# Performance work log

Measured on AMD Instinct MI355X. Metric: run time of the kernel, lower is better.

## Reference

```python
import jax, jax.numpy as jnp
import numpy as np
from jax import lax

PATCH = 16
TAU = 0.5
EPS = 1e-8  # torch CosineSimilarity default eps


def setup_inputs() -> dict:
    key = jax.random.key(0)
    k1, k2, k3, k4, k5 = jax.random.split(key, 5)
    B, C, HW = 64, 3, 384
    hidden, latent = 768, 1024
    return {
        "x": jax.random.normal(k1, (B, C, HW, HW), dtype=jnp.float32),
        "conv_w": jax.random.normal(k2, (hidden, C, PATCH, PATCH), dtype=jnp.float32) * 0.02,
        "conv_b": jax.random.normal(k3, (hidden,), dtype=jnp.float32) * 0.02,
        "latent1": jax.random.normal(k4, (1, latent, hidden), dtype=jnp.float32),
        "latent2": jax.random.normal(k5, (1, latent, hidden), dtype=jnp.float32),
    }


def _cosine_scores(p, p_norm, lat):
    # p: (B, N, D); lat: (L, D) -> (B, N, L) cosine similarity
    l_norm = jnp.linalg.norm(lat, axis=-1)  # (L,)
    dots = jnp.einsum('bnd,ld->bnl', p, lat)
    denom = jnp.maximum(p_norm[:, :, None] * l_norm[None, None, :], EPS)
    return dots / denom


def reference(x, conv_w, conv_b, latent1, latent2):
    # Patch embedding: Conv2d(kernel=stride=16, padding=0)
    patch = lax.conv_general_dilated(
        x, conv_w, window_strides=(PATCH, PATCH), padding='VALID',
        dimension_numbers=('NCHW', 'OIHW', 'NCHW'))
    patch = patch + conv_b[None, :, None, None]  # (B, D, H', W')
    B, D = patch.shape[0], patch.shape[1]
    p = patch.reshape(B, D, -1).transpose(0, 2, 1)  # (B, N, D)
    p_norm = jnp.linalg.norm(p, axis=-1)  # (B, N)

    far = _cosine_scores(p, p_norm, latent1[0])    # (B, N, L)
    close = _cosine_scores(p, p_norm, latent2[0])  # (B, N, L)

    sum_close = jnp.sum(jnp.exp(close / TAU), axis=(1, 2))  # (B,)
    sum_far = jnp.sum(jnp.exp(far / TAU), axis=(1, 2))      # (B,)
    loss = -jnp.log(sum_close / sum_far)
    return loss.mean()
```

## Files before the change

### kernel.cpp

```cpp
#include <hip/hip_runtime.h>
#include <math.h>

using f32x4  = __attribute__((ext_vector_type(4))) float;
using bf16x8 = __attribute__((ext_vector_type(8))) short;

typedef const __attribute__((address_space(1))) void gas_void;
typedef __attribute__((address_space(3))) void las_void;

__device__ __forceinline__ void gl16(const void* g, void* l) {
    __builtin_amdgcn_global_load_lds((gas_void*)g, (las_void*)l, 16, 0, 0);
}

__device__ __forceinline__ unsigned short f2bf(float f) {
    union { float f; unsigned u; } v; v.f = f;
    unsigned r = v.u + 0x7fffu + ((v.u >> 16) & 1u);
    return (unsigned short)(r >> 16);
}
__device__ __forceinline__ float bf2f(unsigned short u) {
    return __uint_as_float(((unsigned)u) << 16);
}

#define VW0() asm volatile("s_waitcnt vmcnt(0)")
#define BAR() __builtin_amdgcn_s_barrier()

__global__ void pcl_prep_wl(const float* __restrict__ w,
                            const float* __restrict__ l1, const float* __restrict__ l2,
                            unsigned short* __restrict__ wsW,
                            unsigned short* __restrict__ wsL) {
    int r = blockIdx.x, t = threadIdx.x;
    if (r < 768) {
        const float* src = w + (size_t)r * 768;
        unsigned short* dst = wsW + (size_t)r * 768;
#pragma unroll
        for (int i = 0; i < 12; ++i) dst[t + 64 * i] = f2bf(src[t + 64 * i]);
    } else {
        int lr = r - 768;
        const float* src = (lr < 1024) ? l1 + (size_t)lr * 768 : l2 + (size_t)(lr - 1024) * 768;
        unsigned short* dst = wsL + (size_t)lr * 768;
        float vals[12];
        float s = 0.f;
#pragma unroll
        for (int i = 0; i < 12; ++i) {
            float f = bf2f(f2bf(src[t + 64 * i]));
            vals[i] = f; s += f * f;
        }
#pragma unroll
        for (int off = 32; off; off >>= 1) s += __shfl_xor(s, off, 64);
        float rn = 1.0f / sqrtf(s);
#pragma unroll
        for (int i = 0; i < 12; ++i) dst[t + 64 * i] = f2bf(vals[i] * rn);
    }
}

#define K1_LDS 108544

__global__ __launch_bounds__(512, 1)
void pcl_k1(const float* __restrict__ x,
            const unsigned short* __restrict__ wsW,
            const float* __restrict__ bias,
            unsigned short* __restrict__ pbuf,
            float* __restrict__ rpn) {
    extern __shared__ char smem[];
    char* AA = smem;
    char* BB = smem + 8192;
    float* nrm = (float*)(smem + 106496);
    const int t = threadIdx.x, w = t >> 6, l = t & 63;
    const size_t Mb = (size_t)blockIdx.x * 64;
    const int ir = l >> 3, s2 = (l & 7) ^ ir;
    const int lm = l & 15, lg4 = l >> 4;

    const int sr = t >> 3, ss = t & 7;
    {
    }
    const int n = (int)Mb + sr;
    const int bb_ = n / 576, n5 = n % 576;
    const int ph = n5 / 24, pw = n5 % 24;
    const float* xbase = x + ((size_t)(bb_ * 3)) * 147456
                       + (size_t)(ph * 16 + (ss >> 1)) * 384 + pw * 16 + (ss & 1) * 8;
    char* aw = AA + sr * 128 + ((ss ^ (sr & 7)) << 4);

    f32x4 acc[4][6];
#pragma unroll
    for (int m = 0; m < 4; ++m)
#pragma unroll
        for (int nf = 0; nf < 6; ++nf) acc[m][nf] = (f32x4)0.f;

    f32x4 xr0, xr1;
    {
        const float* s = xbase;
        xr0 = *(const f32x4*)s; xr1 = *(const f32x4*)(s + 4);
    }

    for (int kc = 0; kc < 12; ++kc) {
        __syncthreads();
#pragma unroll
        for (int rep = 0; rep < 12; ++rep) {
            int c2 = w + 8 * rep;
            gl16(wsW + (size_t)(c2 * 8 + ir) * 768 + kc * 64 + s2 * 8, BB + c2 * 1024);
        }
        {
            bf16x8 pkt;
#pragma unroll
            for (int j = 0; j < 4; ++j) {
                pkt[j]     = (short)f2bf(xr0[j]);
                pkt[4 + j] = (short)f2bf(xr1[j]);
            }
            *(bf16x8*)aw = pkt;
        }
        __syncthreads();

        if (kc < 11) {
            int kn = kc + 1;
            const float* s = xbase + (size_t)(kn >> 2) * 147456 + (kn & 3) * 1536;
            xr0 = *(const f32x4*)s; xr1 = *(const f32x4*)(s + 4);
        }

        bf16x8 a[4][2];
#pragma unroll
        for (int m = 0; m < 4; ++m)
#pragma unroll
            for (int ks = 0; ks < 2; ++ks) {
                int r = m * 16 + lm, slot = ks * 4 + lg4;
                a[m][ks] = *(const bf16x8*)(AA + r * 128 + ((slot ^ (r & 7)) << 4));
            }
#pragma unroll
        for (int nf = 0; nf < 6; ++nf) {
            int rb = w * 96 + nf * 16 + lm;
#pragma unroll
            for (int ks = 0; ks < 2; ++ks) {
                int slot = ks * 4 + lg4;
                bf16x8 bb = *(const bf16x8*)(BB + rb * 128 + ((slot ^ (rb & 7)) << 4));
#pragma unroll
                for (int m = 0; m < 4; ++m)
                    acc[m][nf] = __builtin_amdgcn_mfma_f32_16x16x32_bf16(a[m][ks], bb, acc[m][nf], 0, 0, 0);
            }
        }
    }

    float rs[4][4];
#pragma unroll
    for (int m = 0; m < 4; ++m)
#pragma unroll
        for (int j = 0; j < 4; ++j) rs[m][j] = 0.f;
#pragma unroll
    for (int nf = 0; nf < 6; ++nf) {
        int d = w * 96 + nf * 16 + lm;
        float bv = bias[d];
#pragma unroll
        for (int m = 0; m < 4; ++m)
#pragma unroll
            for (int j = 0; j < 4; ++j) {
                int r = m * 16 + lg4 * 4 + j;
                unsigned short h = f2bf(acc[m][nf][j] + bv);
                pbuf[(Mb + r) * 768 + d] = h;
                float fv = bf2f(h);
                rs[m][j] += fv * fv;
            }
    }
#pragma unroll
    for (int m = 0; m < 4; ++m)
#pragma unroll
        for (int j = 0; j < 4; ++j) {
            rs[m][j] += __shfl_xor(rs[m][j], 1);
            rs[m][j] += __shfl_xor(rs[m][j], 2);
            rs[m][j] += __shfl_xor(rs[m][j], 4);
            rs[m][j] += __shfl_xor(rs[m][j], 8);
        }
    if (lm == 0) {
#pragma unroll
        for (int m = 0; m < 4; ++m)
#pragma unroll
            for (int j = 0; j < 4; ++j)
                nrm[(m * 16 + lg4 * 4 + j) * 8 + w] = rs[m][j];
    }
    __syncthreads();
    if (t < 64) {
        float s = 0.f;
#pragma unroll
        for (int i = 0; i < 8; ++i) s += nrm[t * 8 + i];
        rpn[Mb + t] = 1.0f / sqrtf(s);
    }
}

#define K2_LDS 81920

__global__ __launch_bounds__(256, 2)
void pcl_k2(const unsigned short* __restrict__ pbuf,
            const unsigned short* __restrict__ wsL,
            const float* __restrict__ rpn,
            double* __restrict__ partials) {
    extern __shared__ char smem[];
    const int t = threadIdx.x, w = t >> 6, l = t & 63;
    const int wg = (blockIdx.x & 7) * 384 + (blockIdx.x >> 3);
    const int mt = wg >> 4, nt = wg & 15;
    const size_t Mb = (size_t)mt * 192;
    const int Nb = nt * 128;
    const int wm = w >> 1, wn = w & 1;
    const int ir = l >> 3, s2 = (l & 7) ^ ir;
    const int lm = l & 15, lg4 = l >> 4;

    char* buf0 = smem;
    char* buf1 = smem + 40960;

    auto stage = [&](int kt, char* buf) {
#pragma unroll
        for (int rr = 0; rr < 6; ++rr) {
            int c2 = w * 6 + rr;
            gl16(pbuf + (Mb + c2 * 8 + ir) * 768 + kt * 64 + s2 * 8, buf + c2 * 1024);
        }
#pragma unroll
        for (int rr = 0; rr < 4; ++rr) {
            int c2 = w * 4 + rr;
            gl16(wsL + (size_t)(Nb + c2 * 8 + ir) * 768 + kt * 64 + s2 * 8,
                 buf + 24576 + c2 * 1024);
        }
    };

    f32x4 acc[6][4];
#pragma unroll
    for (int m = 0; m < 6; ++m)
#pragma unroll
        for (int nb = 0; nb < 4; ++nb) acc[m][nb] = (f32x4)0.f;

    stage(0, buf0);
    VW0(); BAR();

    bf16x8 areg[3][2], breg[4][2];

#pragma unroll 2
    for (int kt = 0; kt < 12; ++kt) {
        char* cur = (kt & 1) ? buf1 : buf0;
        char* nxt = (kt & 1) ? buf0 : buf1;

        if (kt < 11) stage(kt + 1, nxt);

#pragma unroll
        for (int nb = 0; nb < 4; ++nb)
#pragma unroll
            for (int ks = 0; ks < 2; ++ks) {
                int rb = wn * 64 + nb * 16 + lm, slot = ks * 4 + lg4;
                breg[nb][ks] = *(const bf16x8*)(cur + 24576 + rb * 128 + ((slot ^ (rb & 7)) << 4));
            }
#pragma unroll
        for (int m = 0; m < 3; ++m)
#pragma unroll
            for (int ks = 0; ks < 2; ++ks) {
                int r = wm * 96 + m * 16 + lm, slot = ks * 4 + lg4;
                areg[m][ks] = *(const bf16x8*)(cur + r * 128 + ((slot ^ (r & 7)) << 4));
            }
        __builtin_amdgcn_s_setprio(1);
#pragma unroll
        for (int m = 0; m < 3; ++m)
#pragma unroll
            for (int nb = 0; nb < 4; ++nb)
#pragma unroll
                for (int ks = 0; ks < 2; ++ks)
                    acc[m][nb] = __builtin_amdgcn_mfma_f32_16x16x32_bf16(areg[m][ks], breg[nb][ks], acc[m][nb], 0, 0, 0);
        __builtin_amdgcn_s_setprio(0);

#pragma unroll
        for (int m = 0; m < 3; ++m)
#pragma unroll
            for (int ks = 0; ks < 2; ++ks) {
                int r = wm * 96 + 48 + m * 16 + lm, slot = ks * 4 + lg4;
                areg[m][ks] = *(const bf16x8*)(cur + r * 128 + ((slot ^ (r & 7)) << 4));
            }
        __builtin_amdgcn_s_setprio(1);
#pragma unroll
        for (int m = 0; m < 3; ++m)
#pragma unroll
            for (int nb = 0; nb < 4; ++nb)
#pragma unroll
                for (int ks = 0; ks < 2; ++ks)
                    acc[3 + m][nb] = __builtin_amdgcn_mfma_f32_16x16x32_bf16(areg[m][ks], breg[nb][ks], acc[3 + m][nb], 0, 0, 0);
        __builtin_amdgcn_s_setprio(0);

        VW0();
        BAR();
    }

    double ssum = 0.0;
#pragma unroll
    for (int m = 0; m < 6; ++m) {
        int mh = m / 3, mi = m % 3;
        int rl = wm * 96 + mh * 48 + mi * 16;
        float rv[4];
#pragma unroll
        for (int j = 0; j < 4; ++j) rv[j] = rpn[Mb + rl + lg4 * 4 + j];
        float es = 0.f;
#pragma unroll
        for (int nb = 0; nb < 4; ++nb)
#pragma unroll
            for (int j = 0; j < 4; ++j)
                es += __expf(2.0f * acc[m][nb][j] * rv[j]);
        ssum += (double)es;
    }
#pragma unroll
    for (int off = 32; off; off >>= 1) ssum += __shfl_down(ssum, off);
    __syncthreads();
    double* red = (double*)smem;
    if (l == 0) red[w] = ssum;
    __syncthreads();
    if (t == 0) {
        double s = 0.0;
#pragma unroll
        for (int i = 0; i < 4; ++i) s += red[i];
        partials[wg] = s;
    }
}

__global__ void pcl_finish(const double* __restrict__ partials, float* __restrict__ out) {
    int b = threadIdx.x;
    double far = 0.0, close = 0.0;
#pragma unroll
    for (int i = 0; i < 3; ++i) {
        int mt = b * 3 + i;
#pragma unroll
        for (int nTile = 0; nTile < 16; ++nTile) {
            double v = partials[mt * 16 + nTile];
            if (nTile < 8) far += v; else close += v;
        }
    }
    double lb = log(far) - log(close);
#pragma unroll
    for (int off = 32; off; off >>= 1) lb += __shfl_down(lb, off);
    if (b == 0) out[0] = (float)(lb * (1.0 / 64.0));
}

extern "C" void kernel_launch(void* const* d_in, const int* in_sizes, int n_in,
                              void* d_out, int out_size, void* d_ws, size_t ws_size,
                              hipStream_t stream) {
    const float* x    = (const float*)d_in[0];
    const float* w    = (const float*)d_in[1];
    const float* bias = (const float*)d_in[2];
    const float* l1   = (const float*)d_in[3];
    const float* l2   = (const float*)d_in[4];
    float* out = (float*)d_out;

    unsigned short* pbuf = (unsigned short*)d_ws;
    unsigned short* wsW  = (unsigned short*)((char*)d_ws + 56623104);
    unsigned short* wsL  = (unsigned short*)((char*)d_ws + 57802752);
    float* rpn           = (float*)((char*)d_ws + 60948480);
    double* partials     = (double*)((char*)d_ws + 61095936);

    (void)hipFuncSetAttribute((const void*)pcl_k1,
                              hipFuncAttributeMaxDynamicSharedMemorySize, K1_LDS);
    (void)hipFuncSetAttribute((const void*)pcl_k2,
                              hipFuncAttributeMaxDynamicSharedMemorySize, K2_LDS);

    pcl_prep_wl<<<2816, 64, 0, stream>>>(w, l1, l2, wsW, wsL);
    pcl_k1<<<576, 512, K1_LDS, stream>>>(x, wsW, bias, pbuf, rpn);
    pcl_k2<<<3072, 256, K2_LDS, stream>>>(pbuf, wsL, rpn, partials);
    pcl_finish<<<1, 64, 0, stream>>>(partials, out);
}
```

Baseline: 216.8 us.

## Retile patch-embed GEMM into 192x128 double-buffered tiles with split norm reduction

The patch-embedding GEMM kernel now uses 192x128 output tiles on 256-thread blocks (two per CU) instead of 64x768 tiles on 512-thread blocks. It double-buffers the A and B tiles in LDS so the next k-step's global loads overlap the current MFMAs, and raises wave priority around the MFMA bursts. Because each block now covers only part of the hidden dimension, per-row squared norms are written as partials and reduced by a new small kernel. The aim is better occupancy and latency hiding for the conversion-heavy fp32 x loads. In exchange, each x element is now read and converted once per column tile (six times), and there is an extra launch.

```diff
diff --git a/kernel.cpp b/kernel.cpp
--- a/kernel.cpp
+++ b/kernel.cpp
@@ -21,6 +21,7 @@
 }
 
 #define VW0() asm volatile("s_waitcnt vmcnt(0)")
+#define VWL0() asm volatile("s_waitcnt vmcnt(0) lgkmcnt(0)")
 #define BAR() __builtin_amdgcn_s_barrier()
 
 __global__ void pcl_prep_wl(const float* __restrict__ w,
@@ -52,113 +53,167 @@
     }
 }
 
-#define K1_LDS 108544
-
-__global__ __launch_bounds__(512, 1)
+#define K1_LDS 81920
+
+__global__ __launch_bounds__(256, 2)
 void pcl_k1(const float* __restrict__ x,
             const unsigned short* __restrict__ wsW,
             const float* __restrict__ bias,
             unsigned short* __restrict__ pbuf,
-            float* __restrict__ rpn) {
+            float* __restrict__ rpnp) {
     extern __shared__ char smem[];
-    char* AA = smem;
-    char* BB = smem + 8192;
-    float* nrm = (float*)(smem + 106496);
     const int t = threadIdx.x, w = t >> 6, l = t & 63;
-    const size_t Mb = (size_t)blockIdx.x * 64;
+    const int wg = (blockIdx.x & 7) * 144 + (blockIdx.x >> 3);
+    const int mt = wg / 6, nt = wg % 6;
+    const size_t Mb = (size_t)mt * 192;
+    const int Nb = nt * 128;
+    const int wm = w >> 1, wn = w & 1;
     const int ir = l >> 3, s2 = (l & 7) ^ ir;
     const int lm = l & 15, lg4 = l >> 4;
 
-    const int sr = t >> 3, ss = t & 7;
-    {
-    }
-    const int n = (int)Mb + sr;
-    const int bb_ = n / 576, n5 = n % 576;
-    const int ph = n5 / 24, pw = n5 % 24;
-    const float* xbase = x + ((size_t)(bb_ * 3)) * 147456
-                       + (size_t)(ph * 16 + (ss >> 1)) * 384 + pw * 16 + (ss & 1) * 8;
-    char* aw = AA + sr * 128 + ((ss ^ (sr & 7)) << 4);
-
-    f32x4 acc[4][6];
-#pragma unroll
-    for (int m = 0; m < 4; ++m)
-#pragma unroll
-        for (int nf = 0; nf < 6; ++nf) acc[m][nf] = (f32x4)0.f;
-
-    f32x4 xr0, xr1;
-    {
-        const float* s = xbase;
-        xr0 = *(const f32x4*)s; xr1 = *(const f32x4*)(s + 4);
-    }
-
-    for (int kc = 0; kc < 12; ++kc) {
-        __syncthreads();
-#pragma unroll
-        for (int rep = 0; rep < 12; ++rep) {
-            int c2 = w + 8 * rep;
-            gl16(wsW + (size_t)(c2 * 8 + ir) * 768 + kc * 64 + s2 * 8, BB + c2 * 1024);
-        }
-        {
+    char* buf0 = smem;
+    char* buf1 = smem + 40960;
+
+    const int sl8 = t & 7;
+    const float* xbase[6];
+    int awoff[6];
+#pragma unroll
+    for (int rep = 0; rep < 6; ++rep) {
+        int row = rep * 32 + (t >> 3);
+        int n = (int)Mb + row;
+        int b = n / 576, n5 = n % 576;
+        int ph = n5 / 24, pw = n5 % 24;
+        xbase[rep] = x + (size_t)b * 442368 + (size_t)ph * 6144 + pw * 16;
+        awoff[rep] = row * 128 + ((sl8 ^ (row & 7)) << 4);
+    }
+    auto xoff = [&](int kt) {
+        int k0 = kt * 64 + sl8 * 8;
+        return (k0 >> 8) * 147456 + (((k0 >> 4) & 15)) * 384 + (k0 & 15);
+    };
+
+    auto issueB = [&](int kt, char* buf) {
+#pragma unroll
+        for (int rr = 0; rr < 4; ++rr) {
+            int c2 = w * 4 + rr;
+            gl16(wsW + (size_t)(Nb + c2 * 8 + ir) * 768 + kt * 64 + s2 * 8,
+                 buf + 24576 + c2 * 1024);
+        }
+    };
+
+    f32x4 xr[6][2];
+    auto loadX = [&](int kt) {
+        int off = xoff(kt);
+#pragma unroll
+        for (int rep = 0; rep < 6; ++rep) {
+            const float* s = xbase[rep] + off;
+            xr[rep][0] = *(const f32x4*)s;
+            xr[rep][1] = *(const f32x4*)(s + 4);
+        }
+    };
+    auto writeA = [&](char* buf) {
+#pragma unroll
+        for (int rep = 0; rep < 6; ++rep) {
             bf16x8 pkt;
 #pragma unroll
             for (int j = 0; j < 4; ++j) {
-                pkt[j]     = (short)f2bf(xr0[j]);
-                pkt[4 + j] = (short)f2bf(xr1[j]);
-            }
-            *(bf16x8*)aw = pkt;
-        }
-        __syncthreads();
-
-        if (kc < 11) {
-            int kn = kc + 1;
-            const float* s = xbase + (size_t)(kn >> 2) * 147456 + (kn & 3) * 1536;
-            xr0 = *(const f32x4*)s; xr1 = *(const f32x4*)(s + 4);
-        }
-
-        bf16x8 a[4][2];
-#pragma unroll
-        for (int m = 0; m < 4; ++m)
-#pragma unroll
-            for (int ks = 0; ks < 2; ++ks) {
-                int r = m * 16 + lm, slot = ks * 4 + lg4;
-                a[m][ks] = *(const bf16x8*)(AA + r * 128 + ((slot ^ (r & 7)) << 4));
-            }
-#pragma unroll
-        for (int nf = 0; nf < 6; ++nf) {
-            int rb = w * 96 + nf * 16 + lm;
-#pragma unroll
-            for (int ks = 0; ks < 2; ++ks) {
-                int slot = ks * 4 + lg4;
-                bf16x8 bb = *(const bf16x8*)(BB + rb * 128 + ((slot ^ (rb & 7)) << 4));
-#pragma unroll
-                for (int m = 0; m < 4; ++m)
-                    acc[m][nf] = __builtin_amdgcn_mfma_f32_16x16x32_bf16(a[m][ks], bb, acc[m][nf], 0, 0, 0);
-            }
-        }
-    }
-
-    float rs[4][4];
-#pragma unroll
-    for (int m = 0; m < 4; ++m)
+                pkt[j]     = (short)f2bf(xr[rep][0][j]);
+                pkt[4 + j] = (short)f2bf(xr[rep][1][j]);
+            }
+            *(bf16x8*)(buf + awoff[rep]) = pkt;
+        }
+    };
+
+    f32x4 acc[6][4];
+#pragma unroll
+    for (int m = 0; m < 6; ++m)
+#pragma unroll
+        for (int nb = 0; nb < 4; ++nb) acc[m][nb] = (f32x4)0.f;
+
+    loadX(0);
+    issueB(0, buf0);
+    writeA(buf0);
+    VWL0(); BAR();
+
+    bf16x8 areg[3][2], breg[4][2];
+
+#pragma unroll 2
+    for (int kt = 0; kt < 12; ++kt) {
+        char* cur = (kt & 1) ? buf1 : buf0;
+        char* nxt = (kt & 1) ? buf0 : buf1;
+
+        if (kt < 11) { loadX(kt + 1); issueB(kt + 1, nxt); }
+
+#pragma unroll
+        for (int nb = 0; nb < 4; ++nb)
+#pragma unroll
+            for (int ks = 0; ks < 2; ++ks) {
+                int rb = wn * 64 + nb * 16 + lm, slot = ks * 4 + lg4;
+                breg[nb][ks] = *(const bf16x8*)(cur + 24576 + rb * 128 + ((slot ^ (rb & 7)) << 4));
+            }
+#pragma unroll
+        for (int m = 0; m < 3; ++m)
+#pragma unroll
+            for (int ks = 0; ks < 2; ++ks) {
+                int r = wm * 96 + m * 16 + lm, slot = ks * 4 + lg4;
+                areg[m][ks] = *(const bf16x8*)(cur + r * 128 + ((slot ^ (r & 7)) << 4));
+            }
+        __builtin_amdgcn_s_setprio(1);
+#pragma unroll
+        for (int m = 0; m < 3; ++m)
+#pragma unroll
+            for (int nb = 0; nb < 4; ++nb)
+#pragma unroll
+                for (int ks = 0; ks < 2; ++ks)
+                    acc[m][nb] = __builtin_amdgcn_mfma_f32_16x16x32_bf16(areg[m][ks], breg[nb][ks], acc[m][nb], 0, 0, 0);
+        __builtin_amdgcn_s_setprio(0);
+
+#pragma unroll
+        for (int m = 0; m < 3; ++m)
+#pragma unroll
+            for (int ks = 0; ks < 2; ++ks) {
+                int r = wm * 96 + 48 + m * 16 + lm, slot = ks * 4 + lg4;
+                areg[m][ks] = *(const bf16x8*)(cur + r * 128 + ((slot ^ (r & 7)) << 4));
+            }
+        __builtin_amdgcn_s_setprio(1);
+#pragma unroll
+        for (int m = 0; m < 3; ++m)
+#pragma unroll
+            for (int nb = 0; nb < 4; ++nb)
+#pragma unroll
+                for (int ks = 0; ks < 2; ++ks)
+                    acc[3 + m][nb] = __builtin_amdgcn_mfma_f32_16x16x32_bf16(areg[m][ks], breg[nb][ks], acc[3 + m][nb], 0, 0, 0);
+        __builtin_amdgcn_s_setprio(0);
+
+        if (kt < 11) writeA(nxt);
+
+        VWL0();
+        BAR();
+    }
+
+    float rs[6][4];
+#pragma unroll
+    for (int m = 0; m < 6; ++m)
 #pragma unroll
         for (int j = 0; j < 4; ++j) rs[m][j] = 0.f;
 #pragma unroll
-    for (int nf = 0; nf < 6; ++nf) {
-        int d = w * 96 + nf * 16 + lm;
+    for (int nb = 0; nb < 4; ++nb) {
+        int d = Nb + wn * 64 + nb * 16 + lm;
         float bv = bias[d];
 #pragma unroll
-        for (int m = 0; m < 4; ++m)
+        for (int m = 0; m < 6; ++m) {
+            int mh = m / 3, mi = m % 3;
 #pragma unroll
             for (int j = 0; j < 4; ++j) {
-                int r = m * 16 + lg4 * 4 + j;
-                unsigned short h = f2bf(acc[m][nf][j] + bv);
-                pbuf[(Mb + r) * 768 + d] = h;
+                int row = wm * 96 + mh * 48 + mi * 16 + lg4 * 4 + j;
+                unsigned short h = f2bf(acc[m][nb][j] + bv);
+                pbuf[(Mb + row) * 768 + d] = h;
                 float fv = bf2f(h);
                 rs[m][j] += fv * fv;
             }
-    }
-#pragma unroll
-    for (int m = 0; m < 4; ++m)
+        }
+    }
+#pragma unroll
+    for (int m = 0; m < 6; ++m)
 #pragma unroll
         for (int j = 0; j < 4; ++j) {
             rs[m][j] += __shfl_xor(rs[m][j], 1);
@@ -166,20 +221,29 @@
             rs[m][j] += __shfl_xor(rs[m][j], 4);
             rs[m][j] += __shfl_xor(rs[m][j], 8);
         }
+    __syncthreads();
+    float* nrm = (float*)smem;
     if (lm == 0) {
 #pragma unroll
-        for (int m = 0; m < 4; ++m)
-#pragma unroll
-            for (int j = 0; j < 4; ++j)
-                nrm[(m * 16 + lg4 * 4 + j) * 8 + w] = rs[m][j];
+        for (int m = 0; m < 6; ++m) {
+            int mh = m / 3, mi = m % 3;
+#pragma unroll
+            for (int j = 0; j < 4; ++j) {
+                int row = wm * 96 + mh * 48 + mi * 16 + lg4 * 4 + j;
+                nrm[row * 2 + wn] = rs[m][j];
+            }
+        }
     }
     __syncthreads();
-    if (t < 64) {
-        float s = 0.f;
-#pragma unroll
-        for (int i = 0; i < 8; ++i) s += nrm[t * 8 + i];
-        rpn[Mb + t] = 1.0f / sqrtf(s);
-    }
+    if (t < 192) rpnp[(size_t)nt * 36864 + Mb + t] = nrm[t * 2] + nrm[t * 2 + 1];
+}
+
+__global__ void pcl_norm(const float* __restrict__ rpnp, float* __restrict__ rpn) {
+    int i = blockIdx.x * 256 + threadIdx.x;
+    float s = 0.f;
+#pragma unroll
+    for (int nt = 0; nt < 6; ++nt) s += rpnp[(size_t)nt * 36864 + i];
+    rpn[i] = 1.0f / sqrtf(s);
 }
 
 #define K2_LDS 81920
@@ -340,8 +404,9 @@
     unsigned short* pbuf = (unsigned short*)d_ws;
     unsigned short* wsW  = (unsigned short*)((char*)d_ws + 56623104);
     unsigned short* wsL  = (unsigned short*)((char*)d_ws + 57802752);
-    float* rpn           = (float*)((char*)d_ws + 60948480);
-    double* partials     = (double*)((char*)d_ws + 61095936);
+    float* rpnp          = (float*)((char*)d_ws + 60948480);
+    float* rpn           = (float*)((char*)d_ws + 61833216);
+    double* partials     = (double*)((char*)d_ws + 61980672);
 
     (void)hipFuncSetAttribute((const void*)pcl_k1,
                               hipFuncAttributeMaxDynamicSharedMemorySize, K1_LDS);
@@ -349,7 +414,8 @@
                               hipFuncAttributeMaxDynamicSharedMemorySize, K2_LDS);
 
     pcl_prep_wl<<<2816, 64, 0, stream>>>(w, l1, l2, wsW, wsL);
-    pcl_k1<<<576, 512, K1_LDS, stream>>>(x, wsW, bias, pbuf, rpn);
+    pcl_k1<<<1152, 256, K1_LDS, stream>>>(x, wsW, bias, pbuf, rpnp);
+    pcl_norm<<<144, 256, 0, stream>>>(rpnp, rpn);
     pcl_k2<<<3072, 256, K2_LDS, stream>>>(pbuf, wsL, rpn, partials);
     pcl_finish<<<1, 64, 0, stream>>>(partials, out);
 }
```

New measurement: 209.9 us. -3.2%, faster.
